# Optimization experiments

Hardware: AMD Instinct MI355X
Metric: run time of the kernel (lower is better)

The kernel has to match this reference:

```python
import jax, jax.numpy as jnp
import numpy as np

B, E, D, V, HW, T = 128, 512, 512, 275, 24, 300


def setup_inputs() -> dict:
    key = jax.random.key(0)
    ks = jax.random.split(key, 24)
    s = 0.05
    feats = jax.random.normal(ks[0], (B, E, HW, HW), jnp.float32)
    captions = jax.random.randint(ks[1], (B, T), 0, V)
    lengths = jax.random.randint(ks[2], (B, 1), 2, T + 1)
    lengths = lengths.at[0, 0].set(T)  # ensure max decode length == T-1 (static)
    def lin(k, fan_in, fan_out):
        return jax.random.normal(k, (fan_in, fan_out), jnp.float32) * s
    return {
        "feats": feats,
        "captions": captions,
        "lengths": lengths,
        "U_w": lin(ks[3], D, D), "U_b": jnp.zeros((D,), jnp.float32),
        "W_w": lin(ks[4], E, D), "W_b": jnp.zeros((D,), jnp.float32),
        "v_w": jax.random.normal(ks[5], (D,), jnp.float32) * s,
        "v_b": jnp.zeros((1,), jnp.float32),
        "init_h_w": lin(ks[6], E, D), "init_h_b": jnp.zeros((D,), jnp.float32),
        "init_c_w": lin(ks[7], E, D), "init_c_b": jnp.zeros((D,), jnp.float32),
        "f_beta_w": lin(ks[8], D, E), "f_beta_b": jnp.zeros((E,), jnp.float32),
        "fc_w": jax.random.uniform(ks[9], (D, V), jnp.float32, -0.1, 0.1),
        "fc_b": jnp.zeros((V,), jnp.float32),
        "emb": jax.random.uniform(ks[10], (V, D), jnp.float32, -0.1, 0.1),
        "lstm_w_ih": jax.random.normal(ks[11], (4 * D, D + E), jnp.float32) * s,
        "lstm_w_hh": jax.random.normal(ks[12], (4 * D, D), jnp.float32) * s,
        "lstm_b_ih": jnp.zeros((4 * D,), jnp.float32),
        "lstm_b_hh": jnp.zeros((4 * D,), jnp.float32),
    }


def reference(feats, captions, lengths, U_w, U_b, W_w, W_b, v_w, v_b,
              init_h_w, init_h_b, init_c_w, init_c_b, f_beta_w, f_beta_b,
              fc_w, fc_b, emb, lstm_w_ih, lstm_w_hh, lstm_b_ih, lstm_b_hh):
    b = feats.shape[0]
    flat = feats.reshape(b, feats.shape[1], -1).transpose(0, 2, 1)  # [B, P, E]
    mean_feats = flat.mean(axis=1)                                   # [B, E]
    h0 = mean_feats @ init_h_w + init_h_b                            # [B, D]
    c0 = mean_feats @ init_c_w + init_c_b
    Ws = flat @ W_w + W_b                                            # [B, P, D] (time-invariant)
    embs = emb[captions]                                             # [B, T, D]
    dec_len = lengths[:, 0] - 1                                      # [B]
    Tm1 = captions.shape[1] - 1
    xs = (embs[:, :Tm1].transpose(1, 0, 2), jnp.arange(Tm1))

    def step(carry, x):
        h, c = carry
        e_t, t = x
        # Bahdanau attention
        att = jnp.tanh(Ws + (h @ U_w + U_b)[:, None, :])             # [B, P, D]
        e = att @ v_w + v_b                                          # [B, P]
        alpha = jax.nn.softmax(e, axis=1)
        ctx = jnp.einsum('bp,bpe->be', alpha, flat)                  # [B, E]
        gate = jax.nn.sigmoid(h @ f_beta_w + f_beta_b)               # [B, E]
        xin = jnp.concatenate([e_t, gate * ctx], axis=1)             # [B, D+E]
        # LSTMCell (torch gate order: i, f, g, o)
        g = xin @ lstm_w_ih.T + lstm_b_ih + h @ lstm_w_hh.T + lstm_b_hh
        i_g, f_g, g_g, o_g = jnp.split(g, 4, axis=1)
        c2 = jax.nn.sigmoid(f_g) * c + jax.nn.sigmoid(i_g) * jnp.tanh(g_g)
        h2 = jax.nn.sigmoid(o_g) * jnp.tanh(c2)
        pred = h2 @ fc_w + fc_b                                      # [B, V]
        m = (dec_len > t)[:, None].astype(pred.dtype)                # active-row mask == torch batch truncation
        return (h2, c2), (pred * m, alpha * m)

    (_, _), (preds, alphas) = jax.lax.scan(step, (h0, c0), xs)
    preds = preds.transpose(1, 0, 2)    # [B, T-1, V]
    alphas = alphas.transpose(1, 0, 2)  # [B, T-1, P]
    return preds, alphas, dec_len
```

## Files before the change

kernel.cpp:

```cpp
#include <hip/hip_runtime.h>
#include <math.h>

static constexpr int Bn  = 128;
static constexpr int En  = 512;
static constexpr int Dn  = 512;
static constexpr int Vn  = 275;
static constexpr int Pn  = 576;
static constexpr int Tn  = 300;
static constexpr int TM1 = 299;

typedef unsigned short ushort_t;
typedef unsigned int uint_t;

__device__ __forceinline__ float fast_tanh(float x) {
    float e2 = __expf(2.0f * x);
    return 1.0f - 2.0f / (e2 + 1.0f);
}
__device__ __forceinline__ float sigmoidf_(float x) {
    return 1.0f / (1.0f + __expf(-x));
}
__device__ __forceinline__ float wave_reduce(float v) {
#pragma unroll
    for (int o = 32; o > 0; o >>= 1) v += __shfl_xor(v, o, 64);
    return v;
}
__device__ __forceinline__ ushort_t f2b(float x) {
    uint_t u = __float_as_uint(x);
    u = (u + 0x7fffu + ((u >> 16) & 1u)) >> 16;
    return (ushort_t)u;
}
__device__ __forceinline__ float b2f(ushort_t u) {
    return __uint_as_float(((uint_t)u) << 16);
}
__device__ __forceinline__ void unpack8(uint4 q, float* f) {
    f[0] = __uint_as_float(q.x << 16); f[1] = __uint_as_float(q.x & 0xffff0000u);
    f[2] = __uint_as_float(q.y << 16); f[3] = __uint_as_float(q.y & 0xffff0000u);
    f[4] = __uint_as_float(q.z << 16); f[5] = __uint_as_float(q.z & 0xffff0000u);
    f[6] = __uint_as_float(q.w << 16); f[7] = __uint_as_float(q.w & 0xffff0000u);
}


__global__ void mean_kernel(const float* __restrict__ feats, float* __restrict__ mean) {
    int w = blockIdx.x * 4 + (threadIdx.x >> 6);
    int lane = threadIdx.x & 63;
    const float* row = feats + (size_t)w * Pn;
    float s = 0.f;
#pragma unroll
    for (int i = 0; i < 9; i++) s += row[lane + i * 64];
    s = wave_reduce(s);
    if (lane == 0) mean[w] = s * (1.0f / Pn);
}

__global__ void init_kernel(const float* __restrict__ mean,
                            const float* __restrict__ ihw, const float* __restrict__ ihb,
                            const float* __restrict__ icw, const float* __restrict__ icb,
                            float* __restrict__ h, float* __restrict__ c) {
    int b = blockIdx.x; int d = threadIdx.x;
    const float* m = mean + b * En;
    float ah = ihb[d], ac = icb[d];
#pragma unroll 8
    for (int e = 0; e < En; e++) {
        float mv = m[e];
        ah += mv * ihw[e * Dn + d];
        ac += mv * icw[e * Dn + d];
    }
    h[b * Dn + d] = ah;
    c[b * Dn + d] = ac;
}

__global__ void ws_kernel(const float* __restrict__ feats, const float* __restrict__ Ww,
                          const float* __restrict__ Wb, ushort_t* __restrict__ WsH) {
    int p = blockIdx.x, b = blockIdx.y, d = threadIdx.x;
    const float* f = feats + (size_t)b * En * Pn + p;
    float acc = Wb[d];
#pragma unroll 8
    for (int e = 0; e < En; e++) acc += f[(size_t)e * Pn] * Ww[e * Dn + d];
    WsH[((size_t)b * Pn + p) * Dn + d] = f2b(acc);
}

__global__ void declen_kernel(const int* __restrict__ lengths, float* __restrict__ out_declen) {
    int b = threadIdx.x;
    if (b < Bn) out_declen[b] = (float)(lengths[b] - 1);
}

__global__ void cvt_kernel(const float* __restrict__ src, ushort_t* __restrict__ dst, int n) {
    int idx = blockIdx.x * 256 + threadIdx.x;
    if (idx < n) dst[idx] = f2b(src[idx]);
}

__global__ void cvtT_kernel(const float* __restrict__ src, ushort_t* __restrict__ dst,
                            int rows, int cols) {
    int idx = blockIdx.x * 256 + threadIdx.x;
    if (idx >= rows * cols) return;
    int r = idx / cols, c = idx - r * cols;
    dst[(size_t)c * rows + r] = f2b(src[idx]);
}


__global__ __launch_bounds__(256) void k16_kernel(
        const float* __restrict__ h,
        const ushort_t* __restrict__ UwTh, const float* __restrict__ Ub,
        const ushort_t* __restrict__ fbwTh, const float* __restrict__ fbb,
        const ushort_t* __restrict__ fcwTh, const float* __restrict__ fcb,
        const int* __restrict__ lengths,
        float* __restrict__ hU, float* __restrict__ gate,
        float* __restrict__ out_preds, int tau) {
    int wid = blockIdx.x * 4 + (threadIdx.x >> 6);
    int lane = threadIdx.x & 63;
    int bg = wid / 325, jg = wid - bg * 325;
    int j0 = jg * 4;
    if (tau == 0 && j0 >= 1024) return;
    const float4* h4 = (const float4*)h;
    float4 hv[4][2];
#pragma unroll
    for (int i = 0; i < 4; i++) {
        int base = (bg * 4 + i) * 128 + 2 * lane;
        hv[i][0] = h4[base]; hv[i][1] = h4[base + 1];
    }
#pragma unroll
    for (int jj = 0; jj < 4; jj++) {
        int j = j0 + jj;
        const ushort_t* row;
        if (j < 512) row = UwTh + (size_t)j * 512;
        else if (j < 1024) row = fbwTh + (size_t)(j - 512) * 512;
        else { if (j - 1024 >= Vn) continue; row = fcwTh + (size_t)(j - 1024) * 512; }
        uint4 q = *(const uint4*)(row + 8 * lane);
        float w8[8]; unpack8(q, w8);
        float a[4];
#pragma unroll
        for (int i = 0; i < 4; i++) {
            a[i] = hv[i][0].x * w8[0] + hv[i][0].y * w8[1] + hv[i][0].z * w8[2] + hv[i][0].w * w8[3]
                 + hv[i][1].x * w8[4] + hv[i][1].y * w8[5] + hv[i][1].z * w8[6] + hv[i][1].w * w8[7];
        }
#pragma unroll
        for (int o = 32; o > 0; o >>= 1) {
#pragma unroll
            for (int i = 0; i < 4; i++) a[i] += __shfl_xor(a[i], o, 64);
        }
        if (lane == 0) {
            if (j < 512) {
                float bias = Ub[j];
#pragma unroll
                for (int i = 0; i < 4; i++) hU[(bg * 4 + i) * Dn + j] = a[i] + bias;
            } else if (j < 1024) {
                int e = j - 512;
                float bias = fbb[e];
#pragma unroll
                for (int i = 0; i < 4; i++) gate[(bg * 4 + i) * En + e] = sigmoidf_(a[i] + bias);
            } else if (tau > 0) {
                int v = j - 1024;
                int t = tau - 1;
                float bias = fcb[v];
#pragma unroll
                for (int i = 0; i < 4; i++) {
                    int b = bg * 4 + i;
                    int dec = lengths[b] - 1;
                    out_preds[((size_t)b * TM1 + t) * Vn + v] = (t < dec) ? (a[i] + bias) : 0.f;
                }
            }
        }
    }
}

__global__ __launch_bounds__(256) void k2_kernel(
        const ushort_t* __restrict__ WsH, const float* __restrict__ hU,
        const float* __restrict__ vw, const float* __restrict__ vb,
        float* __restrict__ esc) {
    int wid = blockIdx.x * 4 + (threadIdx.x >> 6);
    int lane = threadIdx.x & 63;
    int b = wid / Pn;
    const ushort_t* row = WsH + (size_t)wid * Dn;
    uint4 q = *(const uint4*)(row + 8 * lane);
    float w8[8]; unpack8(q, w8);
    const float4* hu4 = (const float4*)(hU + (b << 9));
    float4 h0 = hu4[2 * lane], h1 = hu4[2 * lane + 1];
    const float4* v4 = (const float4*)vw;
    float4 v0 = v4[2 * lane], v1 = v4[2 * lane + 1];
    float acc;
    acc  = fast_tanh(w8[0] + h0.x) * v0.x;
    acc += fast_tanh(w8[1] + h0.y) * v0.y;
    acc += fast_tanh(w8[2] + h0.z) * v0.z;
    acc += fast_tanh(w8[3] + h0.w) * v0.w;
    acc += fast_tanh(w8[4] + h1.x) * v1.x;
    acc += fast_tanh(w8[5] + h1.y) * v1.y;
    acc += fast_tanh(w8[6] + h1.z) * v1.z;
    acc += fast_tanh(w8[7] + h1.w) * v1.w;
    acc = wave_reduce(acc);
    if (lane == 0) esc[wid] = acc + vb[0];
}

__global__ void k3_kernel(const float* __restrict__ esc, float* __restrict__ alpha,
                          float* __restrict__ out_alphas, const int* __restrict__ lengths, int t) {
    __shared__ float red[16];
    int b = blockIdx.x, tid = threadIdx.x;
    int wid = tid >> 6, lane = tid & 63;
    float v = esc[b * Pn + tid];
    float m = v;
#pragma unroll
    for (int o = 32; o > 0; o >>= 1) m = fmaxf(m, __shfl_xor(m, o, 64));
    if (lane == 0) red[wid] = m;
    __syncthreads();
    if (tid == 0) {
        float mm = red[0];
        for (int i = 1; i < 9; i++) mm = fmaxf(mm, red[i]);
        red[9] = mm;
    }
    __syncthreads();
    float mx = red[9];
    float ex = __expf(v - mx);
    float s = ex;
#pragma unroll
    for (int o = 32; o > 0; o >>= 1) s += __shfl_xor(s, o, 64);
    if (lane == 0) red[wid] = s;
    __syncthreads();
    if (tid == 0) {
        float ss = 0.f;
        for (int i = 0; i < 9; i++) ss += red[i];
        red[10] = ss;
    }
    __syncthreads();
    float a = ex / red[10];
    alpha[b * Pn + tid] = a;
    int dec = lengths[b] - 1;
    out_alphas[((size_t)b * TM1 + t) * Pn + tid] = (t < dec) ? a : 0.f;
}

__global__ __launch_bounds__(256) void k4_kernel(
        const ushort_t* __restrict__ featsH, const float* __restrict__ alpha,
        const float* __restrict__ gate, float* __restrict__ xctx) {
    int wid = blockIdx.x * 4 + (threadIdx.x >> 6);
    int lane = threadIdx.x & 63;
    int b = wid >> 9;
    const ushort_t* f = featsH + (size_t)wid * Pn;
    const float* al = alpha + b * Pn;
    uint4 q = *(const uint4*)(f + 8 * lane);
    float w8[8]; unpack8(q, w8);
    const float4* a4 = (const float4*)al;
    float4 a0 = a4[2 * lane], a1 = a4[2 * lane + 1];
    float s;
    s  = w8[0] * a0.x + w8[1] * a0.y + w8[2] * a0.z + w8[3] * a0.w;
    s += w8[4] * a1.x + w8[5] * a1.y + w8[6] * a1.z + w8[7] * a1.w;
    s += b2f(f[512 + lane]) * al[512 + lane];
    s = wave_reduce(s);
    if (lane == 0) xctx[wid] = gate[wid] * s;
}

__global__ __launch_bounds__(256) void k5_kernel(
        const float* __restrict__ h, const float* __restrict__ xctx,
        const float* __restrict__ emb, const int* __restrict__ captions,
        const ushort_t* __restrict__ wihH, const ushort_t* __restrict__ whhH,
        const float* __restrict__ bih, const float* __restrict__ bhh,
        float* __restrict__ c, float* __restrict__ h2, int tau) {
    int wid = blockIdx.x * 4 + (threadIdx.x >> 6);
    int lane = threadIdx.x & 63;
    int bg = wid >> 9, d = wid & 511;
    float4 u[4][6];
#pragma unroll
    for (int i = 0; i < 4; i++) {
        int b = bg * 4 + i;
        int tok = captions[b * Tn + tau];
        const float4* e4 = (const float4*)(emb + (size_t)tok * Dn);
        const float4* x4 = (const float4*)(xctx + b * En);
        const float4* h4 = (const float4*)(h + b * Dn);
        u[i][0] = e4[2 * lane]; u[i][1] = e4[2 * lane + 1];
        u[i][2] = x4[2 * lane]; u[i][3] = x4[2 * lane + 1];
        u[i][4] = h4[2 * lane]; u[i][5] = h4[2 * lane + 1];
    }
    float acc[4][4];
#pragma unroll
    for (int g = 0; g < 4; g++)
#pragma unroll
        for (int i = 0; i < 4; i++) acc[g][i] = 0.f;
#pragma unroll
    for (int g = 0; g < 4; g++) {
        int j = g * 512 + d;
        const ushort_t* wi = wihH + (size_t)j * 1024;
        const ushort_t* wh = whhH + (size_t)j * 512;
        uint4 q0 = *(const uint4*)(wi + 8 * lane);
        uint4 q1 = *(const uint4*)(wi + 512 + 8 * lane);
        uint4 q2 = *(const uint4*)(wh + 8 * lane);
        float wa[8], wb[8], wc[8];
        unpack8(q0, wa); unpack8(q1, wb); unpack8(q2, wc);
#pragma unroll
        for (int i = 0; i < 4; i++) {
            float s;
            s  = u[i][0].x * wa[0] + u[i][0].y * wa[1] + u[i][0].z * wa[2] + u[i][0].w * wa[3];
            s += u[i][1].x * wa[4] + u[i][1].y * wa[5] + u[i][1].z * wa[6] + u[i][1].w * wa[7];
            s += u[i][2].x * wb[0] + u[i][2].y * wb[1] + u[i][2].z * wb[2] + u[i][2].w * wb[3];
            s += u[i][3].x * wb[4] + u[i][3].y * wb[5] + u[i][3].z * wb[6] + u[i][3].w * wb[7];
            s += u[i][4].x * wc[0] + u[i][4].y * wc[1] + u[i][4].z * wc[2] + u[i][4].w * wc[3];
            s += u[i][5].x * wc[4] + u[i][5].y * wc[5] + u[i][5].z * wc[6] + u[i][5].w * wc[7];
            acc[g][i] += s;
        }
    }
#pragma unroll
    for (int o = 32; o > 0; o >>= 1) {
#pragma unroll
        for (int g = 0; g < 4; g++)
#pragma unroll
            for (int i = 0; i < 4; i++) acc[g][i] += __shfl_xor(acc[g][i], o, 64);
    }
    if (lane == 0) {
        float bi = bih[d] + bhh[d];
        float bf = bih[512 + d] + bhh[512 + d];
        float bgg = bih[1024 + d] + bhh[1024 + d];
        float bo = bih[1536 + d] + bhh[1536 + d];
#pragma unroll
        for (int i = 0; i < 4; i++) {
            int b = bg * 4 + i;
            float ig = sigmoidf_(acc[0][i] + bi);
            float fg = sigmoidf_(acc[1][i] + bf);
            float gg = fast_tanh(acc[2][i] + bgg);
            float og = sigmoidf_(acc[3][i] + bo);
            float cn = fg * c[b * Dn + d] + ig * gg;
            c[b * Dn + d] = cn;
            h2[b * Dn + d] = og * fast_tanh(cn);
        }
    }
}

extern "C" void kernel_launch(void* const* d_in, const int* in_sizes, int n_in,
                              void* d_out, int out_size, void* d_ws, size_t ws_size,
                              hipStream_t stream) {
    const float* feats    = (const float*)d_in[0];
    const int*   captions = (const int*)d_in[1];
    const int*   lengths  = (const int*)d_in[2];
    const float* U_w      = (const float*)d_in[3];
    const float* U_b      = (const float*)d_in[4];
    const float* W_w      = (const float*)d_in[5];
    const float* W_b      = (const float*)d_in[6];
    const float* v_w      = (const float*)d_in[7];
    const float* v_b      = (const float*)d_in[8];
    const float* init_h_w = (const float*)d_in[9];
    const float* init_h_b = (const float*)d_in[10];
    const float* init_c_w = (const float*)d_in[11];
    const float* init_c_b = (const float*)d_in[12];
    const float* f_beta_w = (const float*)d_in[13];
    const float* f_beta_b = (const float*)d_in[14];
    const float* fc_w     = (const float*)d_in[15];
    const float* fc_b     = (const float*)d_in[16];
    const float* emb      = (const float*)d_in[17];
    const float* lstm_w_ih = (const float*)d_in[18];
    const float* lstm_w_hh = (const float*)d_in[19];
    const float* lstm_b_ih = (const float*)d_in[20];
    const float* lstm_b_hh = (const float*)d_in[21];

    char* base = (char*)d_ws;
    size_t off = 0;
    ushort_t* WsH    = (ushort_t*)(base + off); off += (size_t)Bn * Pn * Dn * 2;
    ushort_t* featsH = (ushort_t*)(base + off); off += (size_t)Bn * En * Pn * 2;
    ushort_t* wihH   = (ushort_t*)(base + off); off += (size_t)4 * Dn * (Dn + En) * 2;
    ushort_t* whhH   = (ushort_t*)(base + off); off += (size_t)4 * Dn * Dn * 2;
    ushort_t* UwTh   = (ushort_t*)(base + off); off += (size_t)Dn * Dn * 2;
    ushort_t* fbwTh  = (ushort_t*)(base + off); off += (size_t)En * Dn * 2;
    ushort_t* fcwTh  = (ushort_t*)(base + off); off += (size_t)Vn * Dn * 2;
    float* mean  = (float*)(base + off); off += (size_t)Bn * En * 4;
    float* hA    = (float*)(base + off); off += (size_t)Bn * Dn * 4;
    float* hB    = (float*)(base + off); off += (size_t)Bn * Dn * 4;
    float* cbuf  = (float*)(base + off); off += (size_t)Bn * Dn * 4;
    float* hU    = (float*)(base + off); off += (size_t)Bn * Dn * 4;
    float* gate  = (float*)(base + off); off += (size_t)Bn * En * 4;
    float* xctx  = (float*)(base + off); off += (size_t)Bn * En * 4;
    float* esc   = (float*)(base + off); off += (size_t)Bn * Pn * 4;
    float* alpha = (float*)(base + off); off += (size_t)Bn * Pn * 4;

    float* out_preds  = (float*)d_out;
    float* out_alphas = out_preds + (size_t)Bn * TM1 * Vn;
    float* out_declen = out_alphas + (size_t)Bn * TM1 * Pn;

    mean_kernel<<<Bn * En / 4, 256, 0, stream>>>(feats, mean);
    init_kernel<<<Bn, 512, 0, stream>>>(mean, init_h_w, init_h_b, init_c_w, init_c_b, hA, cbuf);
    ws_kernel<<<dim3(Pn, Bn), 512, 0, stream>>>(feats, W_w, W_b, WsH);
    declen_kernel<<<1, 128, 0, stream>>>(lengths, out_declen);
    {
        int n = Bn * En * Pn;
        cvt_kernel<<<(n + 255) / 256, 256, 0, stream>>>(feats, featsH, n);
    }
    cvt_kernel<<<(4 * Dn * (Dn + En) + 255) / 256, 256, 0, stream>>>(lstm_w_ih, wihH, 4 * Dn * (Dn + En));
    cvt_kernel<<<(4 * Dn * Dn + 255) / 256, 256, 0, stream>>>(lstm_w_hh, whhH, 4 * Dn * Dn);
    cvtT_kernel<<<(Dn * Dn + 255) / 256, 256, 0, stream>>>(U_w, UwTh, Dn, Dn);
    cvtT_kernel<<<(Dn * En + 255) / 256, 256, 0, stream>>>(f_beta_w, fbwTh, Dn, En);
    cvtT_kernel<<<(Dn * Vn + 255) / 256, 256, 0, stream>>>(fc_w, fcwTh, Dn, Vn);

    const int k16_blocks = 32 * 325 / 4;
    for (int tau = 0; tau < TM1; tau++) {
        const float* hin = (tau & 1) ? hB : hA;
        float* hout = (tau & 1) ? hA : hB;
        k16_kernel<<<k16_blocks, 256, 0, stream>>>(hin, UwTh, U_b, fbwTh, f_beta_b,
                                                   fcwTh, fc_b, lengths, hU, gate,
                                                   out_preds, tau);
        k2_kernel<<<Bn * Pn / 4, 256, 0, stream>>>(WsH, hU, v_w, v_b, esc);
        k3_kernel<<<Bn, Pn, 0, stream>>>(esc, alpha, out_alphas, lengths, tau);
        k4_kernel<<<Bn * En / 4, 256, 0, stream>>>(featsH, alpha, gate, xctx);
        k5_kernel<<<32 * 512 / 4, 256, 0, stream>>>(hin, xctx, emb, captions,
                                                    wihH, whhH, lstm_b_ih, lstm_b_hh,
                                                    cbuf, hout, tau);
    }
    k16_kernel<<<k16_blocks, 256, 0, stream>>>((TM1 & 1) ? hB : hA, UwTh, U_b, fbwTh, f_beta_b,
                                               fcwTh, fc_b, lengths, hU, gate,
                                               out_preds, TM1);
}
```

Before: 31.92 ms.

## Fuse per-step decode kernels into one persistent cooperative kernel with grid syncs

Replaces the five kernel launches per timestep (about 1500 launches) with a single cooperative persistent kernel. It loops over timesteps and uses grid.sync between phases, fuses the softmax with the context reduction through shared memory, and prefetches rows in the attention-score loop. The aim is to remove launch overhead and the inter-kernel gaps. In exchange, the work runs on only 256 workgroups of 512 threads, and grid-wide barriers add their own latency and can limit memory parallelism in the bandwidth-heavy attention phases.

```diff
diff --git a/kernel.cpp b/kernel.cpp
--- a/kernel.cpp
+++ b/kernel.cpp
@@ -1,5 +1,8 @@
 #include <hip/hip_runtime.h>
+#include <hip/hip_cooperative_groups.h>
 #include <math.h>
+
+namespace cg = cooperative_groups;
 
 static constexpr int Bn  = 128;
 static constexpr int En  = 512;
@@ -8,6 +11,10 @@
 static constexpr int Pn  = 576;
 static constexpr int Tn  = 300;
 static constexpr int TM1 = 299;
+
+static constexpr int NWG    = 256;
+static constexpr int NTHR   = 512;
+static constexpr int NWAVES = NWG * (NTHR / 64);
 
 typedef unsigned short ushort_t;
 typedef unsigned int uint_t;
@@ -97,225 +104,255 @@
 }
 
 
-__global__ __launch_bounds__(256) void k16_kernel(
-        const float* __restrict__ h,
-        const ushort_t* __restrict__ UwTh, const float* __restrict__ Ub,
-        const ushort_t* __restrict__ fbwTh, const float* __restrict__ fbb,
-        const ushort_t* __restrict__ fcwTh, const float* __restrict__ fcb,
-        const int* __restrict__ lengths,
-        float* __restrict__ hU, float* __restrict__ gate,
-        float* __restrict__ out_preds, int tau) {
-    int wid = blockIdx.x * 4 + (threadIdx.x >> 6);
-    int lane = threadIdx.x & 63;
-    int bg = wid / 325, jg = wid - bg * 325;
-    int j0 = jg * 4;
-    if (tau == 0 && j0 >= 1024) return;
-    const float4* h4 = (const float4*)h;
-    float4 hv[4][2];
-#pragma unroll
-    for (int i = 0; i < 4; i++) {
-        int base = (bg * 4 + i) * 128 + 2 * lane;
-        hv[i][0] = h4[base]; hv[i][1] = h4[base + 1];
-    }
-#pragma unroll
-    for (int jj = 0; jj < 4; jj++) {
-        int j = j0 + jj;
-        const ushort_t* row;
-        if (j < 512) row = UwTh + (size_t)j * 512;
-        else if (j < 1024) row = fbwTh + (size_t)(j - 512) * 512;
-        else { if (j - 1024 >= Vn) continue; row = fcwTh + (size_t)(j - 1024) * 512; }
-        uint4 q = *(const uint4*)(row + 8 * lane);
-        float w8[8]; unpack8(q, w8);
-        float a[4];
-#pragma unroll
-        for (int i = 0; i < 4; i++) {
-            a[i] = hv[i][0].x * w8[0] + hv[i][0].y * w8[1] + hv[i][0].z * w8[2] + hv[i][0].w * w8[3]
-                 + hv[i][1].x * w8[4] + hv[i][1].y * w8[5] + hv[i][1].z * w8[6] + hv[i][1].w * w8[7];
+struct LoopParams {
+    const ushort_t* WsH;
+    const ushort_t* featsH;
+    const ushort_t* wihH;
+    const ushort_t* whhH;
+    const ushort_t* UwTh;
+    const ushort_t* fbwTh;
+    const ushort_t* fcwTh;
+    const float* Ub;  const float* fbb; const float* fcb;
+    const float* vw;  const float* vb;
+    const float* bih; const float* bhh;
+    const float* emb;
+    const int* captions; const int* lengths;
+    float* hA; float* hB; float* cbuf;
+    float* hU; float* gate; float* xctx; float* esc;
+    float* out_preds; float* out_alphas;
+};
+
+__global__ __launch_bounds__(NTHR, 2) void loop_kernel(LoopParams p) {
+    cg::grid_group grid = cg::this_grid();
+    const int tid  = threadIdx.x;
+    const int lane = tid & 63;
+    const int wwg  = tid >> 6;
+    const int wg   = blockIdx.x;
+    const int wv   = wg * (NTHR / 64) + wwg;
+
+    __shared__ float s_alpha[Pn];
+    __shared__ float s_red[16];
+
+    for (int tau = 0; tau <= TM1; ++tau) {
+        const float* hin  = (tau & 1) ? p.hB : p.hA;
+        float*       hout = (tau & 1) ? p.hA : p.hB;
+
+        {
+            const float4* h4 = (const float4*)hin;
+            for (int it = wv; it < 32 * 325; it += NWAVES) {
+                int bg = it / 325, jg = it - bg * 325;
+                int j0 = jg * 4;
+                if (tau == 0 && j0 >= 1024) continue;
+                if (tau == TM1 && j0 < 1024) continue;
+                float4 hv[4][2];
+#pragma unroll
+                for (int i = 0; i < 4; i++) {
+                    int basei = (bg * 4 + i) * 128 + 2 * lane;
+                    hv[i][0] = h4[basei]; hv[i][1] = h4[basei + 1];
+                }
+#pragma unroll
+                for (int jj = 0; jj < 4; jj++) {
+                    int j = j0 + jj;
+                    const ushort_t* row;
+                    if (j < 512) row = p.UwTh + (size_t)j * 512;
+                    else if (j < 1024) row = p.fbwTh + (size_t)(j - 512) * 512;
+                    else { if (j - 1024 >= Vn) continue; row = p.fcwTh + (size_t)(j - 1024) * 512; }
+                    uint4 q = *(const uint4*)(row + 8 * lane);
+                    float w8[8]; unpack8(q, w8);
+                    float a[4];
+#pragma unroll
+                    for (int i = 0; i < 4; i++) {
+                        a[i] = hv[i][0].x * w8[0] + hv[i][0].y * w8[1] + hv[i][0].z * w8[2] + hv[i][0].w * w8[3]
+                             + hv[i][1].x * w8[4] + hv[i][1].y * w8[5] + hv[i][1].z * w8[6] + hv[i][1].w * w8[7];
+                    }
+#pragma unroll
+                    for (int o = 32; o > 0; o >>= 1) {
+#pragma unroll
+                        for (int i = 0; i < 4; i++) a[i] += __shfl_xor(a[i], o, 64);
+                    }
+                    if (lane == 0) {
+                        if (j < 512) {
+                            float bias = p.Ub[j];
+#pragma unroll
+                            for (int i = 0; i < 4; i++) p.hU[(bg * 4 + i) * Dn + j] = a[i] + bias;
+                        } else if (j < 1024) {
+                            int e = j - 512;
+                            float bias = p.fbb[e];
+#pragma unroll
+                            for (int i = 0; i < 4; i++) p.gate[(bg * 4 + i) * En + e] = sigmoidf_(a[i] + bias);
+                        } else if (tau > 0) {
+                            int v = j - 1024;
+                            int t = tau - 1;
+                            float bias = p.fcb[v];
+#pragma unroll
+                            for (int i = 0; i < 4; i++) {
+                                int b = bg * 4 + i;
+                                int dec = p.lengths[b] - 1;
+                                p.out_preds[((size_t)b * TM1 + t) * Vn + v] = (t < dec) ? (a[i] + bias) : 0.f;
+                            }
+                        }
+                    }
+                }
+            }
         }
-#pragma unroll
-        for (int o = 32; o > 0; o >>= 1) {
-#pragma unroll
-            for (int i = 0; i < 4; i++) a[i] += __shfl_xor(a[i], o, 64);
+        if (tau == TM1) break;
+        grid.sync();
+
+        {
+            int b  = wv >> 4;
+            int p0 = (wv & 15) * 36;
+            const float4* hu4 = (const float4*)(p.hU + (b << 9));
+            float4 h0 = hu4[2 * lane], h1 = hu4[2 * lane + 1];
+            const float4* v4 = (const float4*)p.vw;
+            float4 vv0 = v4[2 * lane], vv1 = v4[2 * lane + 1];
+            float vb0 = p.vb[0];
+            const ushort_t* base = p.WsH + ((size_t)b * Pn + p0) * Dn + 8 * lane;
+            uint4 q = *(const uint4*)base;
+            for (int k = 0; k < 36; ++k) {
+                uint4 qn = q;
+                if (k < 35) qn = *(const uint4*)(base + (size_t)(k + 1) * Dn);
+                float w8[8]; unpack8(q, w8);
+                float acc;
+                acc  = fast_tanh(w8[0] + h0.x) * vv0.x;
+                acc += fast_tanh(w8[1] + h0.y) * vv0.y;
+                acc += fast_tanh(w8[2] + h0.z) * vv0.z;
+                acc += fast_tanh(w8[3] + h0.w) * vv0.w;
+                acc += fast_tanh(w8[4] + h1.x) * vv1.x;
+                acc += fast_tanh(w8[5] + h1.y) * vv1.y;
+                acc += fast_tanh(w8[6] + h1.z) * vv1.z;
+                acc += fast_tanh(w8[7] + h1.w) * vv1.w;
+                acc = wave_reduce(acc);
+                if (lane == 0) p.esc[b * Pn + p0 + k] = acc + vb0;
+                q = qn;
+            }
         }
-        if (lane == 0) {
-            if (j < 512) {
-                float bias = Ub[j];
-#pragma unroll
-                for (int i = 0; i < 4; i++) hU[(bg * 4 + i) * Dn + j] = a[i] + bias;
-            } else if (j < 1024) {
-                int e = j - 512;
-                float bias = fbb[e];
-#pragma unroll
-                for (int i = 0; i < 4; i++) gate[(bg * 4 + i) * En + e] = sigmoidf_(a[i] + bias);
-            } else if (tau > 0) {
-                int v = j - 1024;
-                int t = tau - 1;
-                float bias = fcb[v];
+        grid.sync();
+
+        {
+            int b = wg >> 1, half = wg & 1;
+            float v0 = p.esc[b * Pn + tid];
+            float v1 = (tid < 64) ? p.esc[b * Pn + 512 + tid] : -3.0e38f;
+            float m = fmaxf(v0, v1);
+#pragma unroll
+            for (int o = 32; o > 0; o >>= 1) m = fmaxf(m, __shfl_xor(m, o, 64));
+            if (lane == 0) s_red[wwg] = m;
+            __syncthreads();
+            if (tid == 0) {
+                float mm = s_red[0];
+                for (int i = 1; i < 8; i++) mm = fmaxf(mm, s_red[i]);
+                s_red[8] = mm;
+            }
+            __syncthreads();
+            float mx  = s_red[8];
+            float ex0 = __expf(v0 - mx);
+            float ex1 = (tid < 64) ? __expf(v1 - mx) : 0.f;
+            float ssum = wave_reduce(ex0 + ex1);
+            if (lane == 0) s_red[wwg] = ssum;
+            __syncthreads();
+            if (tid == 0) {
+                float ss = 0.f;
+                for (int i = 0; i < 8; i++) ss += s_red[i];
+                s_red[9] = 1.0f / ss;
+            }
+            __syncthreads();
+            float inv = s_red[9];
+            float a0 = ex0 * inv;
+            float a1 = ex1 * inv;
+            s_alpha[tid] = a0;
+            if (tid < 64) s_alpha[512 + tid] = a1;
+            if (half == 0) {
+                int dec = p.lengths[b] - 1;
+                float keep = (tau < dec) ? 1.f : 0.f;
+                size_t rb = ((size_t)b * TM1 + tau) * Pn;
+                p.out_alphas[rb + tid] = a0 * keep;
+                if (tid < 64) p.out_alphas[rb + 512 + tid] = a1 * keep;
+            }
+            __syncthreads();
+            const float4* a4 = (const float4*)s_alpha;
+            float4 aa0 = a4[2 * lane], aa1 = a4[2 * lane + 1];
+            float atail = s_alpha[512 + lane];
+            for (int r = wwg; r < 256; r += 8) {
+                int e = half * 256 + r;
+                const ushort_t* f = p.featsH + ((size_t)(b * En + e)) * Pn;
+                uint4 q = *(const uint4*)(f + 8 * lane);
+                float w8[8]; unpack8(q, w8);
+                float s;
+                s  = w8[0] * aa0.x + w8[1] * aa0.y + w8[2] * aa0.z + w8[3] * aa0.w;
+                s += w8[4] * aa1.x + w8[5] * aa1.y + w8[6] * aa1.z + w8[7] * aa1.w;
+                s += b2f(f[512 + lane]) * atail;
+                s = wave_reduce(s);
+                if (lane == 0) p.xctx[b * En + e] = p.gate[b * En + e] * s;
+            }
+        }
+        grid.sync();
+
+        for (int it = wv; it < 32 * 512; it += NWAVES) {
+            int bg = it >> 9, d = it & 511;
+            float4 u[4][6];
+#pragma unroll
+            for (int i = 0; i < 4; i++) {
+                int b = bg * 4 + i;
+                int tok = p.captions[b * Tn + tau];
+                const float4* e4 = (const float4*)(p.emb + (size_t)tok * Dn);
+                const float4* x4 = (const float4*)(p.xctx + b * En);
+                const float4* h4 = (const float4*)(hin + b * Dn);
+                u[i][0] = e4[2 * lane]; u[i][1] = e4[2 * lane + 1];
+                u[i][2] = x4[2 * lane]; u[i][3] = x4[2 * lane + 1];
+                u[i][4] = h4[2 * lane]; u[i][5] = h4[2 * lane + 1];
+            }
+            float acc[4][4];
+#pragma unroll
+            for (int g = 0; g < 4; g++)
+#pragma unroll
+                for (int i = 0; i < 4; i++) acc[g][i] = 0.f;
+#pragma unroll
+            for (int g = 0; g < 4; g++) {
+                int j = g * 512 + d;
+                const ushort_t* wi = p.wihH + (size_t)j * 1024;
+                const ushort_t* wh = p.whhH + (size_t)j * 512;
+                uint4 q0 = *(const uint4*)(wi + 8 * lane);
+                uint4 q1 = *(const uint4*)(wi + 512 + 8 * lane);
+                uint4 q2 = *(const uint4*)(wh + 8 * lane);
+                float wa[8], wb[8], wc[8];
+                unpack8(q0, wa); unpack8(q1, wb); unpack8(q2, wc);
+#pragma unroll
+                for (int i = 0; i < 4; i++) {
+                    float s;
+                    s  = u[i][0].x * wa[0] + u[i][0].y * wa[1] + u[i][0].z * wa[2] + u[i][0].w * wa[3];
+                    s += u[i][1].x * wa[4] + u[i][1].y * wa[5] + u[i][1].z * wa[6] + u[i][1].w * wa[7];
+                    s += u[i][2].x * wb[0] + u[i][2].y * wb[1] + u[i][2].z * wb[2] + u[i][2].w * wb[3];
+                    s += u[i][3].x * wb[4] + u[i][3].y * wb[5] + u[i][3].z * wb[6] + u[i][3].w * wb[7];
+                    s += u[i][4].x * wc[0] + u[i][4].y * wc[1] + u[i][4].z * wc[2] + u[i][4].w * wc[3];
+                    s += u[i][5].x * wc[4] + u[i][5].y * wc[5] + u[i][5].z * wc[6] + u[i][5].w * wc[7];
+                    acc[g][i] += s;
+                }
+            }
+#pragma unroll
+            for (int o = 32; o > 0; o >>= 1) {
+#pragma unroll
+                for (int g = 0; g < 4; g++)
+#pragma unroll
+                    for (int i = 0; i < 4; i++) acc[g][i] += __shfl_xor(acc[g][i], o, 64);
+            }
+            if (lane == 0) {
+                float bi  = p.bih[d] + p.bhh[d];
+                float bf  = p.bih[512 + d] + p.bhh[512 + d];
+                float bgg = p.bih[1024 + d] + p.bhh[1024 + d];
+                float bo  = p.bih[1536 + d] + p.bhh[1536 + d];
 #pragma unroll
                 for (int i = 0; i < 4; i++) {
                     int b = bg * 4 + i;
-                    int dec = lengths[b] - 1;
-                    out_preds[((size_t)b * TM1 + t) * Vn + v] = (t < dec) ? (a[i] + bias) : 0.f;
+                    float ig = sigmoidf_(acc[0][i] + bi);
+                    float fg = sigmoidf_(acc[1][i] + bf);
+                    float gg = fast_tanh(acc[2][i] + bgg);
+                    float og = sigmoidf_(acc[3][i] + bo);
+                    float cn = fg * p.cbuf[b * Dn + d] + ig * gg;
+                    p.cbuf[b * Dn + d] = cn;
+                    hout[b * Dn + d] = og * fast_tanh(cn);
                 }
             }
         }
-    }
-}
-
-__global__ __launch_bounds__(256) void k2_kernel(
-        const ushort_t* __restrict__ WsH, const float* __restrict__ hU,
-        const float* __restrict__ vw, const float* __restrict__ vb,
-        float* __restrict__ esc) {
-    int wid = blockIdx.x * 4 + (threadIdx.x >> 6);
-    int lane = threadIdx.x & 63;
-    int b = wid / Pn;
-    const ushort_t* row = WsH + (size_t)wid * Dn;
-    uint4 q = *(const uint4*)(row + 8 * lane);
-    float w8[8]; unpack8(q, w8);
-    const float4* hu4 = (const float4*)(hU + (b << 9));
-    float4 h0 = hu4[2 * lane], h1 = hu4[2 * lane + 1];
-    const float4* v4 = (const float4*)vw;
-    float4 v0 = v4[2 * lane], v1 = v4[2 * lane + 1];
-    float acc;
-    acc  = fast_tanh(w8[0] + h0.x) * v0.x;
-    acc += fast_tanh(w8[1] + h0.y) * v0.y;
-    acc += fast_tanh(w8[2] + h0.z) * v0.z;
-    acc += fast_tanh(w8[3] + h0.w) * v0.w;
-    acc += fast_tanh(w8[4] + h1.x) * v1.x;
-    acc += fast_tanh(w8[5] + h1.y) * v1.y;
-    acc += fast_tanh(w8[6] + h1.z) * v1.z;
-    acc += fast_tanh(w8[7] + h1.w) * v1.w;
-    acc = wave_reduce(acc);
-    if (lane == 0) esc[wid] = acc + vb[0];
-}
-
-__global__ void k3_kernel(const float* __restrict__ esc, float* __restrict__ alpha,
-                          float* __restrict__ out_alphas, const int* __restrict__ lengths, int t) {
-    __shared__ float red[16];
-    int b = blockIdx.x, tid = threadIdx.x;
-    int wid = tid >> 6, lane = tid & 63;
-    float v = esc[b * Pn + tid];
-    float m = v;
-#pragma unroll
-    for (int o = 32; o > 0; o >>= 1) m = fmaxf(m, __shfl_xor(m, o, 64));
-    if (lane == 0) red[wid] = m;
-    __syncthreads();
-    if (tid == 0) {
-        float mm = red[0];
-        for (int i = 1; i < 9; i++) mm = fmaxf(mm, red[i]);
-        red[9] = mm;
-    }
-    __syncthreads();
-    float mx = red[9];
-    float ex = __expf(v - mx);
-    float s = ex;
-#pragma unroll
-    for (int o = 32; o > 0; o >>= 1) s += __shfl_xor(s, o, 64);
-    if (lane == 0) red[wid] = s;
-    __syncthreads();
-    if (tid == 0) {
-        float ss = 0.f;
-        for (int i = 0; i < 9; i++) ss += red[i];
-        red[10] = ss;
-    }
-    __syncthreads();
-    float a = ex / red[10];
-    alpha[b * Pn + tid] = a;
-    int dec = lengths[b] - 1;
-    out_alphas[((size_t)b * TM1 + t) * Pn + tid] = (t < dec) ? a : 0.f;
-}
-
-__global__ __launch_bounds__(256) void k4_kernel(
-        const ushort_t* __restrict__ featsH, const float* __restrict__ alpha,
-        const float* __restrict__ gate, float* __restrict__ xctx) {
-    int wid = blockIdx.x * 4 + (threadIdx.x >> 6);
-    int lane = threadIdx.x & 63;
-    int b = wid >> 9;
-    const ushort_t* f = featsH + (size_t)wid * Pn;
-    const float* al = alpha + b * Pn;
-    uint4 q = *(const uint4*)(f + 8 * lane);
-    float w8[8]; unpack8(q, w8);
-    const float4* a4 = (const float4*)al;
-    float4 a0 = a4[2 * lane], a1 = a4[2 * lane + 1];
-    float s;
-    s  = w8[0] * a0.x + w8[1] * a0.y + w8[2] * a0.z + w8[3] * a0.w;
-    s += w8[4] * a1.x + w8[5] * a1.y + w8[6] * a1.z + w8[7] * a1.w;
-    s += b2f(f[512 + lane]) * al[512 + lane];
-    s = wave_reduce(s);
-    if (lane == 0) xctx[wid] = gate[wid] * s;
-}
-
-__global__ __launch_bounds__(256) void k5_kernel(
-        const float* __restrict__ h, const float* __restrict__ xctx,
-        const float* __restrict__ emb, const int* __restrict__ captions,
-        const ushort_t* __restrict__ wihH, const ushort_t* __restrict__ whhH,
-        const float* __restrict__ bih, const float* __restrict__ bhh,
-        float* __restrict__ c, float* __restrict__ h2, int tau) {
-    int wid = blockIdx.x * 4 + (threadIdx.x >> 6);
-    int lane = threadIdx.x & 63;
-    int bg = wid >> 9, d = wid & 511;
-    float4 u[4][6];
-#pragma unroll
-    for (int i = 0; i < 4; i++) {
-        int b = bg * 4 + i;
-        int tok = captions[b * Tn + tau];
-        const float4* e4 = (const float4*)(emb + (size_t)tok * Dn);
-        const float4* x4 = (const float4*)(xctx + b * En);
-        const float4* h4 = (const float4*)(h + b * Dn);
-        u[i][0] = e4[2 * lane]; u[i][1] = e4[2 * lane + 1];
-        u[i][2] = x4[2 * lane]; u[i][3] = x4[2 * lane + 1];
-        u[i][4] = h4[2 * lane]; u[i][5] = h4[2 * lane + 1];
-    }
-    float acc[4][4];
-#pragma unroll
-    for (int g = 0; g < 4; g++)
-#pragma unroll
-        for (int i = 0; i < 4; i++) acc[g][i] = 0.f;
-#pragma unroll
-    for (int g = 0; g < 4; g++) {
-        int j = g * 512 + d;
-        const ushort_t* wi = wihH + (size_t)j * 1024;
-        const ushort_t* wh = whhH + (size_t)j * 512;
-        uint4 q0 = *(const uint4*)(wi + 8 * lane);
-        uint4 q1 = *(const uint4*)(wi + 512 + 8 * lane);
-        uint4 q2 = *(const uint4*)(wh + 8 * lane);
-        float wa[8], wb[8], wc[8];
-        unpack8(q0, wa); unpack8(q1, wb); unpack8(q2, wc);
-#pragma unroll
-        for (int i = 0; i < 4; i++) {
-            float s;
-            s  = u[i][0].x * wa[0] + u[i][0].y * wa[1] + u[i][0].z * wa[2] + u[i][0].w * wa[3];
-            s += u[i][1].x * wa[4] + u[i][1].y * wa[5] + u[i][1].z * wa[6] + u[i][1].w * wa[7];
-            s += u[i][2].x * wb[0] + u[i][2].y * wb[1] + u[i][2].z * wb[2] + u[i][2].w * wb[3];
-            s += u[i][3].x * wb[4] + u[i][3].y * wb[5] + u[i][3].z * wb[6] + u[i][3].w * wb[7];
-            s += u[i][4].x * wc[0] + u[i][4].y * wc[1] + u[i][4].z * wc[2] + u[i][4].w * wc[3];
-            s += u[i][5].x * wc[4] + u[i][5].y * wc[5] + u[i][5].z * wc[6] + u[i][5].w * wc[7];
-            acc[g][i] += s;
-        }
-    }
-#pragma unroll
-    for (int o = 32; o > 0; o >>= 1) {
-#pragma unroll
-        for (int g = 0; g < 4; g++)
-#pragma unroll
-            for (int i = 0; i < 4; i++) acc[g][i] += __shfl_xor(acc[g][i], o, 64);
-    }
-    if (lane == 0) {
-        float bi = bih[d] + bhh[d];
-        float bf = bih[512 + d] + bhh[512 + d];
-        float bgg = bih[1024 + d] + bhh[1024 + d];
-        float bo = bih[1536 + d] + bhh[1536 + d];
-#pragma unroll
-        for (int i = 0; i < 4; i++) {
-            int b = bg * 4 + i;
-            float ig = sigmoidf_(acc[0][i] + bi);
-            float fg = sigmoidf_(acc[1][i] + bf);
-            float gg = fast_tanh(acc[2][i] + bgg);
-            float og = sigmoidf_(acc[3][i] + bo);
-            float cn = fg * c[b * Dn + d] + ig * gg;
-            c[b * Dn + d] = cn;
-            h2[b * Dn + d] = og * fast_tanh(cn);
-        }
+        grid.sync();
     }
 }
 
@@ -362,7 +399,6 @@
     float* gate  = (float*)(base + off); off += (size_t)Bn * En * 4;
     float* xctx  = (float*)(base + off); off += (size_t)Bn * En * 4;
     float* esc   = (float*)(base + off); off += (size_t)Bn * Pn * 4;
-    float* alpha = (float*)(base + off); off += (size_t)Bn * Pn * 4;
 
     float* out_preds  = (float*)d_out;
     float* out_alphas = out_preds + (size_t)Bn * TM1 * Vn;
@@ -382,21 +418,19 @@
     cvtT_kernel<<<(Dn * En + 255) / 256, 256, 0, stream>>>(f_beta_w, fbwTh, Dn, En);
     cvtT_kernel<<<(Dn * Vn + 255) / 256, 256, 0, stream>>>(fc_w, fcwTh, Dn, Vn);
 
-    const int k16_blocks = 32 * 325 / 4;
-    for (int tau = 0; tau < TM1; tau++) {
-        const float* hin = (tau & 1) ? hB : hA;
-        float* hout = (tau & 1) ? hA : hB;
-        k16_kernel<<<k16_blocks, 256, 0, stream>>>(hin, UwTh, U_b, fbwTh, f_beta_b,
-                                                   fcwTh, fc_b, lengths, hU, gate,
-                                                   out_preds, tau);
-        k2_kernel<<<Bn * Pn / 4, 256, 0, stream>>>(WsH, hU, v_w, v_b, esc);
-        k3_kernel<<<Bn, Pn, 0, stream>>>(esc, alpha, out_alphas, lengths, tau);
-        k4_kernel<<<Bn * En / 4, 256, 0, stream>>>(featsH, alpha, gate, xctx);
-        k5_kernel<<<32 * 512 / 4, 256, 0, stream>>>(hin, xctx, emb, captions,
-                                                    wihH, whhH, lstm_b_ih, lstm_b_hh,
-                                                    cbuf, hout, tau);
-    }
-    k16_kernel<<<k16_blocks, 256, 0, stream>>>((TM1 & 1) ? hB : hA, UwTh, U_b, fbwTh, f_beta_b,
-                                               fcwTh, fc_b, lengths, hU, gate,
-                                               out_preds, TM1);
-}
+    LoopParams lp;
+    lp.WsH = WsH; lp.featsH = featsH; lp.wihH = wihH; lp.whhH = whhH;
+    lp.UwTh = UwTh; lp.fbwTh = fbwTh; lp.fcwTh = fcwTh;
+    lp.Ub = U_b; lp.fbb = f_beta_b; lp.fcb = fc_b;
+    lp.vw = v_w; lp.vb = v_b;
+    lp.bih = lstm_b_ih; lp.bhh = lstm_b_hh;
+    lp.emb = emb;
+    lp.captions = captions; lp.lengths = lengths;
+    lp.hA = hA; lp.hB = hB; lp.cbuf = cbuf;
+    lp.hU = hU; lp.gate = gate; lp.xctx = xctx; lp.esc = esc;
+    lp.out_preds = out_preds; lp.out_alphas = out_alphas;
+
+    void* kargs[] = { (void*)&lp };
+    hipLaunchCooperativeKernel((const void*)loop_kernel, dim3(NWG), dim3(NTHR),
+                               kargs, 0, stream);
+}
```

Measured after the change: 70.97 ms. +122.3%, slower.
